# Optimization experiments

Measured on AMD Instinct MI355X. Metric: run time of the kernel, lower is better.

## Reference

```python
import jax, jax.numpy as jnp
import numpy as np

N, M, E, DIM = 100000, 2000, 400000, 128
GIN = 2 * DIM + 3  # gate MLP input width


def _mlp2(x, W1, b1, W2, b2):
    # Linear -> ReLU -> Linear
    return jnp.maximum(x @ W1 + b1, 0.0) @ W2 + b2


def setup_inputs() -> dict:
    key = jax.random.key(0)
    ks = jax.random.split(key, 20)
    s = lambda fan_in: 1.0 / np.sqrt(fan_in)
    inp = {
        "res_feat": jax.random.normal(ks[0], (N, DIM), jnp.float32),
        "meta_feat": jax.random.normal(ks[1], (M, DIM), jnp.float32),
        "sec_ids": jax.random.randint(ks[2], (N,), 0, M),
        "batch_pe_vector": jax.random.normal(ks[3], (N, 3), jnp.float32),
        "batch_meta_2_node_edge": jax.random.randint(ks[4], (2, E), 0, M),
        "batch_meta_2_node_vector": jax.random.normal(ks[5], (E, 3), jnp.float32),
        # gate1 params
        "g1_W1": jax.random.uniform(ks[6], (GIN, DIM), jnp.float32, -s(GIN), s(GIN)),
        "g1_b1": jnp.zeros((DIM,), jnp.float32),
        "g1_W2": jax.random.uniform(ks[7], (DIM, DIM), jnp.float32, -s(DIM), s(DIM)),
        "g1_b2": jnp.zeros((DIM,), jnp.float32),
        # gate2 params
        "g2_W1": jax.random.uniform(ks[8], (GIN, DIM), jnp.float32, -s(GIN), s(GIN)),
        "g2_b1": jnp.zeros((DIM,), jnp.float32),
        "g2_W2": jax.random.uniform(ks[9], (DIM, DIM), jnp.float32, -s(DIM), s(DIM)),
        "g2_b2": jnp.zeros((DIM,), jnp.float32),
        # fuse params
        "f_W1": jax.random.uniform(ks[10], (DIM, DIM), jnp.float32, -s(DIM), s(DIM)),
        "f_b1": jnp.zeros((DIM,), jnp.float32),
        "f_W2": jax.random.uniform(ks[11], (DIM, DIM), jnp.float32, -s(DIM), s(DIM)),
        "f_b2": jnp.zeros((DIM,), jnp.float32),
    }
    return inp


def reference(res_feat, meta_feat, sec_ids, batch_pe_vector,
              batch_meta_2_node_edge, batch_meta_2_node_vector,
              g1_W1, g1_b1, g1_W2, g1_b2,
              g2_W1, g2_b1, g2_W2, g2_b2,
              f_W1, f_b1, f_W2, f_b2):
    n = res_feat.shape[0]
    # gate1: per-node gather of meta features
    meta_broadcast = meta_feat[sec_ids]                       # [N, dim]
    gate1_in = jnp.concatenate([res_feat, meta_broadcast, -batch_pe_vector], axis=-1)
    gate1_w = _mlp2(gate1_in, g1_W1, g1_b1, g1_W2, g1_b2)     # [N, dim]
    # gate2: per-edge gathers
    src, dst = batch_meta_2_node_edge[0], batch_meta_2_node_edge[1]
    meta_add = meta_feat[src]                                 # [E, dim]
    res_b = res_feat[dst]                                     # [E, dim]
    gate2_in = jnp.concatenate([res_b, meta_add, batch_meta_2_node_vector], axis=-1)
    gate2_w = _mlp2(gate2_in, g2_W1, g2_b1, g2_W2, g2_b2)     # [E, dim]
    # scatter_mean over destination nodes
    vals = gate2_w * meta_add
    sums = jax.ops.segment_sum(vals, dst, num_segments=n)
    cnts = jax.ops.segment_sum(jnp.ones((vals.shape[0],), vals.dtype), dst, num_segments=n)
    meta_add_fea = sums / jnp.maximum(cnts, 1.0)[:, None]
    fused = res_feat + gate1_w * meta_broadcast + meta_add_fea
    return _mlp2(fused, f_W1, f_b1, f_W2, f_b2)
```

## Files before the change

kernel.cpp:

```cpp
#include <hip/hip_runtime.h>


typedef short bf16x8 __attribute__((ext_vector_type(8)));
typedef float f32x4  __attribute__((ext_vector_type(4)));

#define XS_PAD 136
#define S_SPLIT 4

__device__ __forceinline__ unsigned short f2bf(float f){
  union { float f; unsigned u; } v; v.f = f;
  return (unsigned short)((v.u + 0x7FFFu + ((v.u >> 16) & 1u)) >> 16);
}
__device__ __forceinline__ unsigned pack2(float a, float b){
  return (unsigned)f2bf(a) | ((unsigned)f2bf(b) << 16);
}
__device__ __forceinline__ float bf2f(unsigned short u){
  union { unsigned u; float f; } v; v.u = ((unsigned)u) << 16; return v.f;
}

__device__ __forceinline__ void mfma_layer(const unsigned short* Xs,
                                           const bf16x8 (&B)[2][4],
                                           int lane, f32x4 (&acc)[4][2]) {
  const int lcol = lane & 15, quad = lane >> 4;
  #pragma unroll
  for (int rg = 0; rg < 4; ++rg) {
    bf16x8 A[4];
    const unsigned short* ab = Xs + (rg*16 + lcol)*XS_PAD + quad*8;
    #pragma unroll
    for (int kk = 0; kk < 4; ++kk) A[kk] = *(const bf16x8*)(ab + kk*32);
    #pragma unroll
    for (int ctl = 0; ctl < 2; ++ctl)
      #pragma unroll
      for (int kk = 0; kk < 4; ++kk)
        acc[rg][ctl] = __builtin_amdgcn_mfma_f32_16x16x32_bf16(
            A[kk], B[ctl][kk], acc[rg][ctl], 0, 0, 0);
  }
}

__device__ __forceinline__ void load_bfrags(const unsigned short* __restrict__ Wt,
                                            int wave, int lane, bf16x8 (&B)[2][4]) {
  const int lcol = lane & 15, quad = lane >> 4;
  #pragma unroll
  for (int ctl = 0; ctl < 2; ++ctl) {
    int col = (wave*2 + ctl)*16 + lcol;
    #pragma unroll
    for (int kk = 0; kk < 4; ++kk)
      B[ctl][kk] = *(const bf16x8*)(Wt + (size_t)col*128 + kk*32 + quad*8);
  }
}

__device__ __forceinline__ void zero_acc(f32x4 (&acc)[4][2]) {
  #pragma unroll
  for (int rg = 0; rg < 4; ++rg)
    #pragma unroll
    for (int ctl = 0; ctl < 2; ++ctl) {
      acc[rg][ctl][0]=0.f; acc[rg][ctl][1]=0.f;
      acc[rg][ctl][2]=0.f; acc[rg][ctl][3]=0.f;
    }
}

struct WPtrs { const float* s[8]; };
__global__ __launch_bounds__(256) void transpose_w8(WPtrs p,
                                                    unsigned short* __restrict__ dstbase) {
  int slab = blockIdx.x >> 4, blk = blockIdx.x & 15;
  const float* W = p.s[slab];
  unsigned short* Wt = dstbase + (size_t)slab*16384;
  int c  = blk*8 + (threadIdx.x >> 5);
  int k0 = (threadIdx.x & 31) * 4;
  unsigned short o[4];
  #pragma unroll
  for (int j = 0; j < 4; ++j) o[j] = f2bf(W[(size_t)(k0 + j)*128 + c]);
  *(uint2*)(Wt + (size_t)c*128 + k0) =
      make_uint2((unsigned)o[0] | ((unsigned)o[1] << 16),
                 (unsigned)o[2] | ((unsigned)o[3] << 16));
}

__global__ __launch_bounds__(256) void prep_mfma(const float* __restrict__ res,
                                                 const float* __restrict__ meta,
                                                 const unsigned short* __restrict__ WAt,
                                                 const unsigned short* __restrict__ WBt,
                                                 float* __restrict__ A2,
                                                 float* __restrict__ M2, int mrows) {
  __shared__ __align__(16) unsigned short Xs[64*XS_PAD];
  const int t = threadIdx.x, lane = t & 63, wave = t >> 6;
  const int quad = lane >> 4, lcol = lane & 15;
  const int tile0 = blockIdx.x * 64;
  const float* X = blockIdx.y ? meta : res;
  const unsigned short* Wt = blockIdx.y ? WBt : WAt;
  float* Y = blockIdx.y ? M2 : A2;
  bf16x8 B[2][4];
  load_bfrags(Wt, wave, lane, B);
  #pragma unroll
  for (int i = 0; i < 8; ++i) {
    int f = t + i*256, row = f >> 5, c4 = f & 31;
    int gr = tile0 + row;
    float4 v = make_float4(0.f,0.f,0.f,0.f);
    if (gr < mrows) v = *(const float4*)(X + (size_t)gr*128 + c4*4);
    *(uint2*)(Xs + row*XS_PAD + c4*4) = make_uint2(pack2(v.x,v.y), pack2(v.z,v.w));
  }
  __syncthreads();
  f32x4 acc[4][2]; zero_acc(acc);
  mfma_layer(Xs, B, lane, acc);
  #pragma unroll
  for (int rg = 0; rg < 4; ++rg)
    #pragma unroll
    for (int ctl = 0; ctl < 2; ++ctl) {
      int col = (wave*2 + ctl)*16 + lcol;
      #pragma unroll
      for (int reg = 0; reg < 4; ++reg) {
        int gr = tile0 + rg*16 + quad*4 + reg;
        if (gr < mrows) Y[(size_t)gr*128 + col] = acc[rg][ctl][reg];
      }
    }
}

__global__ void hist_kernel(const int* __restrict__ dst, int* __restrict__ counts, int E){
  int e = blockIdx.x*256 + threadIdx.x;
  if (e < E) atomicAdd(&counts[dst[e]], 1);
}
__global__ void scan1(const int* __restrict__ counts, int* __restrict__ exoff,
                      int* __restrict__ blocksum, int N){
  __shared__ int s[256];
  int t = threadIdx.x, gid = blockIdx.x*256 + t;
  int v = (gid < N) ? counts[gid] : 0;
  s[t] = v; __syncthreads();
  for (int off = 1; off < 256; off <<= 1){
    int x = (t >= off) ? s[t-off] : 0; __syncthreads();
    s[t] += x; __syncthreads();
  }
  if (gid < N) exoff[gid] = s[t] - v;
  if (t == 255) blocksum[blockIdx.x] = s[255];
}
__global__ void scan2(int* __restrict__ blocksum, int nb){
  __shared__ int s[512];
  int t = threadIdx.x;
  int v = (t < nb) ? blocksum[t] : 0;
  s[t] = v; __syncthreads();
  for (int off = 1; off < 512; off <<= 1){
    int x = (t >= off) ? s[t-off] : 0; __syncthreads();
    s[t] += x; __syncthreads();
  }
  if (t < nb) blocksum[t] = s[t] - v;
}
__global__ void scan3(int* __restrict__ exoff, const int* __restrict__ blockbase,
                      int* __restrict__ cursor, int N){
  int gid = blockIdx.x*256 + threadIdx.x;
  if (gid < N){ int v = exoff[gid] + blockbase[gid >> 8]; exoff[gid] = v; cursor[gid] = v; }
}
__global__ void fill_kernel(const int* __restrict__ dst, int* __restrict__ cursor,
                            int* __restrict__ edge_ids, int E){
  int e = blockIdx.x*256 + threadIdx.x;
  if (e < E){ int p = atomicAdd(&cursor[dst[e]], 1); edge_ids[p] = e; }
}

__global__ __launch_bounds__(256) void edge_mfma(
    const float* __restrict__ A2, const float* __restrict__ M2,
    const float* __restrict__ meta, const float* __restrict__ evec,
    const int* __restrict__ src, const int* __restrict__ edge_ids,
    const int* __restrict__ row_start, const int* __restrict__ counts,
    const float* __restrict__ b1, const float* __restrict__ g2W1full,
    const unsigned short* __restrict__ W2t, const float* __restrict__ b2,
    float* __restrict__ SUM) {
  const int n = blockIdx.x / S_SPLIT, k = blockIdx.x % S_SPLIT;
  const int count = counts[n];
  const int per = (count + S_SPLIT - 1) / S_SPLIT;
  const int lo = k * per;
  int hi = lo + per; if (hi > count) hi = count;
  const int cnt = hi - lo;
  if (cnt <= 0) return;
  const int rs = row_start[n] + lo;

  __shared__ __align__(16) unsigned short Xh[64*XS_PAD];
  __shared__ int srcl[64];
  __shared__ float evl[64*3];
  const int t = threadIdx.x, lane = t & 63, wave = t >> 6;
  const int quad = lane >> 4, lcol = lane & 15;
  const int c0 = (t & 31) * 4, rbase = t >> 5;

  bf16x8 BW2[2][4];
  load_bfrags(W2t, wave, lane, BW2);
  float4 a2v = *(const float4*)(A2 + (size_t)n*128 + c0);
  float4 b1v = *(const float4*)(b1 + c0);
  float4 base = make_float4(a2v.x+b1v.x, a2v.y+b1v.y, a2v.z+b1v.z, a2v.w+b1v.w);
  float4 w0 = *(const float4*)(g2W1full + 256*128 + c0);
  float4 w1 = *(const float4*)(g2W1full + 257*128 + c0);
  float4 w2 = *(const float4*)(g2W1full + 258*128 + c0);
  const int colA = wave*32 + lcol, colB = colA + 16;
  const float b2A = b2[colA], b2B = b2[colB];
  float psA = 0.f, psB = 0.f;

  for (int t0 = 0; t0 < cnt; t0 += 64) {
    __syncthreads();
    if (t < 64) {
      int idx = t0 + t;
      int s = 0; float e0=0.f,e1=0.f,e2=0.f;
      if (idx < cnt) {
        int e = edge_ids[rs + idx];
        s = src[e];
        e0 = evec[(size_t)e*3]; e1 = evec[(size_t)e*3+1]; e2 = evec[(size_t)e*3+2];
      }
      srcl[t] = s; evl[t*3] = e0; evl[t*3+1] = e1; evl[t*3+2] = e2;
    }
    __syncthreads();
    #pragma unroll
    for (int i = 0; i < 8; ++i) {
      int row = rbase + 8*i;
      float4 h = make_float4(0.f,0.f,0.f,0.f);
      if (t0 + row < cnt) {
        int s = srcl[row];
        float4 m = *(const float4*)(M2 + (size_t)s*128 + c0);
        float e0 = evl[row*3], e1 = evl[row*3+1], e2 = evl[row*3+2];
        h.x = fmaxf(base.x + m.x + e0*w0.x + e1*w1.x + e2*w2.x, 0.f);
        h.y = fmaxf(base.y + m.y + e0*w0.y + e1*w1.y + e2*w2.y, 0.f);
        h.z = fmaxf(base.z + m.z + e0*w0.z + e1*w1.z + e2*w2.z, 0.f);
        h.w = fmaxf(base.w + m.w + e0*w0.w + e1*w1.w + e2*w2.w, 0.f);
      }
      *(uint2*)(Xh + row*XS_PAD + c0) = make_uint2(pack2(h.x,h.y), pack2(h.z,h.w));
    }
    __syncthreads();
    f32x4 acc[4][2]; zero_acc(acc);
    mfma_layer(Xh, BW2, lane, acc);
    #pragma unroll
    for (int rg = 0; rg < 4; ++rg)
      #pragma unroll
      for (int reg = 0; reg < 4; ++reg) {
        int rl = rg*16 + quad*4 + reg;
        if (t0 + rl < cnt) {
          int s = srcl[rl];
          psA += (acc[rg][0][reg] + b2A) * meta[(size_t)s*128 + colA];
          psB += (acc[rg][1][reg] + b2B) * meta[(size_t)s*128 + colB];
        }
      }
  }
  psA += __shfl_xor(psA, 16, 64); psA += __shfl_xor(psA, 32, 64);
  psB += __shfl_xor(psB, 16, 64); psB += __shfl_xor(psB, 32, 64);
  if (quad == 0) {
    atomicAdd(&SUM[(size_t)n*128 + colA], psA);
    atomicAdd(&SUM[(size_t)n*128 + colB], psB);
  }
}

__global__ __launch_bounds__(256) void fused_node(
    const float* __restrict__ res, const float* __restrict__ meta,
    const int* __restrict__ sec_ids, const float* __restrict__ pe,
    const float* __restrict__ g1W1full,
    const unsigned short* __restrict__ g1At, const unsigned short* __restrict__ g1Bt,
    const unsigned short* __restrict__ g1W2t, const float* __restrict__ g1b1,
    const float* __restrict__ g1b2,
    const unsigned short* __restrict__ fW1t, const float* __restrict__ fb1v,
    const unsigned short* __restrict__ fW2t, const float* __restrict__ fb2v,
    const float* __restrict__ SUM, const int* __restrict__ counts, int msize,
    float* __restrict__ out, int rows) {
  __shared__ __align__(16) unsigned short Xa[64*XS_PAD];
  __shared__ __align__(16) unsigned short Xm[64*XS_PAD];
  __shared__ int   sids[64];
  __shared__ float pel[64*3];
  __shared__ float inv[64];
  const int t = threadIdx.x, lane = t & 63, wave = t >> 6;
  const int quad = lane >> 4, lcol = lane & 15;
  const int tile0 = blockIdx.x * 64;
  const int c0 = (t & 31) * 4, rbase = t >> 5;

  if (t < 64) {
    int gr = tile0 + t;
    sids[t] = (gr < rows) ? sec_ids[gr] : 0;
    float p0=0.f,p1=0.f,p2=0.f;
    if (gr < rows){ p0=pe[(size_t)gr*3]; p1=pe[(size_t)gr*3+1]; p2=pe[(size_t)gr*3+2]; }
    pel[t*3]=p0; pel[t*3+1]=p1; pel[t*3+2]=p2;
    int c = (gr < rows && gr < msize) ? counts[gr] : 0;
    inv[t] = (c > 0) ? 1.f/(float)c : 0.f;
  }
  const int colA = wave*32 + lcol, colB = colA + 16;
  const float b1A = g1b1[colA],  b1B = g1b1[colB];
  const float b2A = g1b2[colA],  b2B = g1b2[colB];
  const float fb1A = fb1v[colA], fb1B = fb1v[colB];
  const float fb2A = fb2v[colA], fb2B = fb2v[colB];
  const float wA0 = g1W1full[256*128+colA], wA1 = g1W1full[257*128+colA],
              wA2 = g1W1full[258*128+colA];
  const float wB0 = g1W1full[256*128+colB], wB1 = g1W1full[257*128+colB],
              wB2 = g1W1full[258*128+colB];
  bf16x8 BA[2][4], BB[2][4];
  load_bfrags(g1At, wave, lane, BA);
  load_bfrags(g1Bt, wave, lane, BB);
  __syncthreads();

  #pragma unroll
  for (int i = 0; i < 8; ++i) {
    int row = rbase + 8*i;
    int gr = tile0 + row;
    float4 rv = make_float4(0.f,0.f,0.f,0.f);
    float4 mv = make_float4(0.f,0.f,0.f,0.f);
    if (gr < rows) {
      rv = *(const float4*)(res  + (size_t)gr*128 + c0);
      mv = *(const float4*)(meta + (size_t)sids[row]*128 + c0);
    }
    *(uint2*)(Xa + row*XS_PAD + c0) = make_uint2(pack2(rv.x,rv.y), pack2(rv.z,rv.w));
    *(uint2*)(Xm + row*XS_PAD + c0) = make_uint2(pack2(mv.x,mv.y), pack2(mv.z,mv.w));
  }
  __syncthreads();

  f32x4 acc[4][2]; zero_acc(acc);
  mfma_layer(Xa, BA, lane, acc);
  mfma_layer(Xm, BB, lane, acc);
  __syncthreads();
  #pragma unroll
  for (int rg = 0; rg < 4; ++rg)
    #pragma unroll
    for (int reg = 0; reg < 4; ++reg) {
      int row = rg*16 + quad*4 + reg;
      float p0 = pel[row*3], p1 = pel[row*3+1], p2 = pel[row*3+2];
      float vA = acc[rg][0][reg] + b1A - p0*wA0 - p1*wA1 - p2*wA2;
      float vB = acc[rg][1][reg] + b1B - p0*wB0 - p1*wB1 - p2*wB2;
      Xa[row*XS_PAD + colA] = f2bf(fmaxf(vA, 0.f));
      Xa[row*XS_PAD + colB] = f2bf(fmaxf(vB, 0.f));
    }
  __syncthreads();
  bf16x8 B2g[2][4]; load_bfrags(g1W2t, wave, lane, B2g);
  zero_acc(acc);
  mfma_layer(Xa, B2g, lane, acc);
  __syncthreads();
  #pragma unroll
  for (int rg = 0; rg < 4; ++rg)
    #pragma unroll
    for (int reg = 0; reg < 4; ++reg) {
      int row = rg*16 + quad*4 + reg;
      Xa[row*XS_PAD + colA] = f2bf(acc[rg][0][reg] + b2A);
      Xa[row*XS_PAD + colB] = f2bf(acc[rg][1][reg] + b2B);
    }
  __syncthreads();
  #pragma unroll
  for (int i = 0; i < 8; ++i) {
    int row = rbase + 8*i;
    int gr = tile0 + row;
    if (gr < rows) {
      float4 rv = *(const float4*)(res + (size_t)gr*128 + c0);
      uint2 gu = *(const uint2*)(Xa + row*XS_PAD + c0);
      uint2 mu = *(const uint2*)(Xm + row*XS_PAD + c0);
      float g0 = bf2f((unsigned short)(gu.x & 0xFFFF)), g1 = bf2f((unsigned short)(gu.x >> 16));
      float g2 = bf2f((unsigned short)(gu.y & 0xFFFF)), g3 = bf2f((unsigned short)(gu.y >> 16));
      float m0 = bf2f((unsigned short)(mu.x & 0xFFFF)), m1 = bf2f((unsigned short)(mu.x >> 16));
      float m2 = bf2f((unsigned short)(mu.y & 0xFFFF)), m3 = bf2f((unsigned short)(mu.y >> 16));
      float iv = inv[row];
      float s0=0.f,s1=0.f,s2=0.f,s3=0.f;
      if (iv > 0.f) {
        float4 s = *(const float4*)(SUM + (size_t)gr*128 + c0);
        s0 = s.x*iv; s1 = s.y*iv; s2 = s.z*iv; s3 = s.w*iv;
      }
      float f0 = rv.x + g0*m0 + s0, f1 = rv.y + g1*m1 + s1;
      float f2v = rv.z + g2*m2 + s2, f3 = rv.w + g3*m3 + s3;
      *(uint2*)(Xm + row*XS_PAD + c0) = make_uint2(pack2(f0,f1), pack2(f2v,f3));
    }
  }
  __syncthreads();
  bf16x8 BF1[2][4]; load_bfrags(fW1t, wave, lane, BF1);
  zero_acc(acc);
  mfma_layer(Xm, BF1, lane, acc);
  #pragma unroll
  for (int rg = 0; rg < 4; ++rg)
    #pragma unroll
    for (int reg = 0; reg < 4; ++reg) {
      int row = rg*16 + quad*4 + reg;
      Xa[row*XS_PAD + colA] = f2bf(fmaxf(acc[rg][0][reg] + fb1A, 0.f));
      Xa[row*XS_PAD + colB] = f2bf(fmaxf(acc[rg][1][reg] + fb1B, 0.f));
    }
  __syncthreads();
  bf16x8 BF2[2][4]; load_bfrags(fW2t, wave, lane, BF2);
  zero_acc(acc);
  mfma_layer(Xa, BF2, lane, acc);
  #pragma unroll
  for (int rg = 0; rg < 4; ++rg)
    #pragma unroll
    for (int reg = 0; reg < 4; ++reg) {
      int gr = tile0 + rg*16 + quad*4 + reg;
      if (gr < rows) {
        out[(size_t)gr*128 + colA] = acc[rg][0][reg] + fb2A;
        out[(size_t)gr*128 + colB] = acc[rg][1][reg] + fb2B;
      }
    }
}

extern "C" void kernel_launch(void* const* d_in, const int* in_sizes, int n_in,
                              void* d_out, int out_size, void* d_ws, size_t ws_size,
                              hipStream_t stream) {
  const float* res     = (const float*)d_in[0];
  const float* meta    = (const float*)d_in[1];
  const int*   sec_ids = (const int*)  d_in[2];
  const float* pe      = (const float*)d_in[3];
  const int*   edge    = (const int*)  d_in[4];
  const float* evec    = (const float*)d_in[5];
  const float* g1W1 = (const float*)d_in[6];
  const float* g1b1 = (const float*)d_in[7];
  const float* g1W2 = (const float*)d_in[8];
  const float* g1b2 = (const float*)d_in[9];
  const float* g2W1 = (const float*)d_in[10];
  const float* g2b1 = (const float*)d_in[11];
  const float* g2W2 = (const float*)d_in[12];
  const float* g2b2 = (const float*)d_in[13];
  const float* fW1  = (const float*)d_in[14];
  const float* fb1  = (const float*)d_in[15];
  const float* fW2  = (const float*)d_in[16];
  const float* fb2  = (const float*)d_in[17];

  const int N = in_sizes[0] / 128;
  const int M = in_sizes[1] / 128;
  const int E = in_sizes[4] / 2;
  const int* src = edge;
  const int* dst = edge + E;

  float* ws = (float*)d_ws;
  float* A2   = ws;
  float* M2   = A2 + (size_t)M*128;
  float* SUMb = M2 + (size_t)M*128;
  int* counts     = (int*)(SUMb + (size_t)M*128);
  int* row_startp = counts + M;
  int* cursor     = row_startp + M;
  int* blocksum   = cursor + M;
  int* edge_ids   = blocksum + 512;
  uintptr_t wp = (uintptr_t)(edge_ids + E);
  wp = (wp + 15) & ~(uintptr_t)15;
  unsigned short* Wt = (unsigned short*)wp;
  unsigned short* W_g1A  = Wt + 0*16384;
  unsigned short* W_g1B  = Wt + 1*16384;
  unsigned short* W_g1W2 = Wt + 2*16384;
  unsigned short* W_g2A  = Wt + 3*16384;
  unsigned short* W_g2B  = Wt + 4*16384;
  unsigned short* W_g2W2 = Wt + 5*16384;
  unsigned short* W_fW1  = Wt + 6*16384;
  unsigned short* W_fW2  = Wt + 7*16384;
  float* out = (float*)d_out;

  hipMemsetAsync(counts, 0, (size_t)M*sizeof(int), stream);
  hipMemsetAsync(SUMb, 0, (size_t)M*128*sizeof(float), stream);

  WPtrs p;
  p.s[0] = g1W1;            p.s[1] = g1W1 + 128*128;  p.s[2] = g1W2;
  p.s[3] = g2W1;            p.s[4] = g2W1 + 128*128;  p.s[5] = g2W2;
  p.s[6] = fW1;             p.s[7] = fW2;
  transpose_w8<<<128, 256, 0, stream>>>(p, Wt);

  const int nbMt = (M + 63) / 64;
  const int nbN  = (N + 63) / 64;
  const int nbE  = (E + 255) / 256;
  const int nbS  = (M + 255) / 256;

  prep_mfma<<<dim3(nbMt, 2), 256, 0, stream>>>(res, meta, W_g2A, W_g2B, A2, M2, M);

  hist_kernel<<<nbE, 256, 0, stream>>>(dst, counts, E);
  scan1<<<nbS, 256, 0, stream>>>(counts, row_startp, blocksum, M);
  scan2<<<1, 512, 0, stream>>>(blocksum, nbS);
  scan3<<<nbS, 256, 0, stream>>>(row_startp, blocksum, cursor, M);
  fill_kernel<<<nbE, 256, 0, stream>>>(dst, cursor, edge_ids, E);

  edge_mfma<<<M*S_SPLIT, 256, 0, stream>>>(A2, M2, meta, evec, src, edge_ids,
                                           row_startp, counts, g2b1, g2W1,
                                           W_g2W2, g2b2, SUMb);

  fused_node<<<nbN, 256, 0, stream>>>(res, meta, sec_ids, pe, g1W1,
                                      W_g1A, W_g1B, W_g1W2, g1b1, g1b2,
                                      W_fW1, fb1, W_fW2, fb2,
                                      SUMb, counts, M, out, N);
}
```

Measured before the change: 396.3 us.

## Merge launches, pack edge data in CSR fill, and shrink fused_node LDS

The memsets are folded into the weight-transpose kernel, the prep GEMM and histogram run in one launch, and the three-kernel scan becomes a single-block scan, which cuts launch count. The fill kernel now writes src index and edge vector as a packed float4 in CSR order, so edge_mfma drops the edge_ids indirection and prefetches the next tile's edge data. fused_node uses one LDS tile instead of two and loads weight fragments as needed, aiming for lower LDS and register use and higher occupancy. The cost is that the epilogue rereads meta, res and SUM from global memory with scattered scalar loads.

```diff
diff --git a/kernel.cpp b/kernel.cpp
--- a/kernel.cpp
+++ b/kernel.cpp
@@ -13,9 +13,6 @@
 }
 __device__ __forceinline__ unsigned pack2(float a, float b){
   return (unsigned)f2bf(a) | ((unsigned)f2bf(b) << 16);
-}
-__device__ __forceinline__ float bf2f(unsigned short u){
-  union { unsigned u; float f; } v; v.u = ((unsigned)u) << 16; return v.f;
 }
 
 __device__ __forceinline__ void mfma_layer(const unsigned short* Xs,
@@ -61,7 +58,9 @@
 
 struct WPtrs { const float* s[8]; };
 __global__ __launch_bounds__(256) void transpose_w8(WPtrs p,
-                                                    unsigned short* __restrict__ dstbase) {
+                                                    unsigned short* __restrict__ dstbase,
+                                                    float* __restrict__ SUM,
+                                                    int* __restrict__ counts, int M) {
   int slab = blockIdx.x >> 4, blk = blockIdx.x & 15;
   const float* W = p.s[slab];
   unsigned short* Wt = dstbase + (size_t)slab*16384;
@@ -73,21 +72,34 @@
   *(uint2*)(Wt + (size_t)c*128 + k0) =
       make_uint2((unsigned)o[0] | ((unsigned)o[1] << 16),
                  (unsigned)o[2] | ((unsigned)o[3] << 16));
-}
-
-__global__ __launch_bounds__(256) void prep_mfma(const float* __restrict__ res,
-                                                 const float* __restrict__ meta,
-                                                 const unsigned short* __restrict__ WAt,
-                                                 const unsigned short* __restrict__ WBt,
-                                                 float* __restrict__ A2,
-                                                 float* __restrict__ M2, int mrows) {
+  int tid = blockIdx.x*256 + threadIdx.x;
+  int tot = gridDim.x*256;
+  float4 z = make_float4(0.f,0.f,0.f,0.f);
+  for (int i = tid; i < M*32; i += tot) ((float4*)SUM)[i] = z;
+  for (int i = tid; i < M; i += tot) counts[i] = 0;
+}
+
+__global__ __launch_bounds__(256) void prep_and_hist(
+    const float* __restrict__ res, const float* __restrict__ meta,
+    const unsigned short* __restrict__ WAt, const unsigned short* __restrict__ WBt,
+    const float* __restrict__ b1,
+    float* __restrict__ A2, float* __restrict__ M2, int mrows, int nbPrep,
+    const int* __restrict__ dst, int* __restrict__ counts, int E) {
+  if ((int)blockIdx.x >= nbPrep) {
+    int e = ((int)blockIdx.x - nbPrep)*256 + threadIdx.x;
+    if (e < E) atomicAdd(&counts[dst[e]], 1);
+    return;
+  }
   __shared__ __align__(16) unsigned short Xs[64*XS_PAD];
   const int t = threadIdx.x, lane = t & 63, wave = t >> 6;
   const int quad = lane >> 4, lcol = lane & 15;
-  const int tile0 = blockIdx.x * 64;
-  const float* X = blockIdx.y ? meta : res;
-  const unsigned short* Wt = blockIdx.y ? WBt : WAt;
-  float* Y = blockIdx.y ? M2 : A2;
+  const int half = nbPrep >> 1;
+  const int yy = ((int)blockIdx.x >= half) ? 1 : 0;
+  const int bx = (int)blockIdx.x - yy*half;
+  const int tile0 = bx * 64;
+  const float* X = yy ? meta : res;
+  const unsigned short* Wt = yy ? WBt : WAt;
+  float* Y = yy ? M2 : A2;
   bf16x8 B[2][4];
   load_bfrags(Wt, wave, lane, B);
   #pragma unroll
@@ -106,59 +118,60 @@
     #pragma unroll
     for (int ctl = 0; ctl < 2; ++ctl) {
       int col = (wave*2 + ctl)*16 + lcol;
+      float badd = 0.f;
+      if (!yy) badd = b1[col];
       #pragma unroll
       for (int reg = 0; reg < 4; ++reg) {
         int gr = tile0 + rg*16 + quad*4 + reg;
-        if (gr < mrows) Y[(size_t)gr*128 + col] = acc[rg][ctl][reg];
+        if (gr < mrows) Y[(size_t)gr*128 + col] = acc[rg][ctl][reg] + badd;
       }
     }
 }
 
-__global__ void hist_kernel(const int* __restrict__ dst, int* __restrict__ counts, int E){
+__global__ __launch_bounds__(1024) void scan_all(const int* __restrict__ counts,
+                                                 int* __restrict__ row_start,
+                                                 int* __restrict__ cursor, int M) {
+  __shared__ int s[1024];
+  __shared__ int carry_s;
+  const int t = threadIdx.x;
+  if (t == 0) carry_s = 0;
+  __syncthreads();
+  for (int base = 0; base < M; base += 2048) {
+    int i0 = base + 2*t, i1 = i0 + 1;
+    int c0 = (i0 < M) ? counts[i0] : 0;
+    int c1 = (i1 < M) ? counts[i1] : 0;
+    int pair = c0 + c1;
+    s[t] = pair; __syncthreads();
+    for (int off = 1; off < 1024; off <<= 1) {
+      int x = (t >= off) ? s[t-off] : 0; __syncthreads();
+      s[t] += x; __syncthreads();
+    }
+    int carry = carry_s;
+    int excl = carry + s[t] - pair;
+    if (i0 < M) { row_start[i0] = excl;       cursor[i0] = excl; }
+    if (i1 < M) { row_start[i1] = excl + c0;  cursor[i1] = excl + c0; }
+    __syncthreads();
+    if (t == 1023) carry_s = carry + s[1023];
+    __syncthreads();
+  }
+}
+
+__global__ void fill_kernel(const int* __restrict__ dst, const int* __restrict__ src,
+                            const float* __restrict__ evec, int* __restrict__ cursor,
+                            float4* __restrict__ edata, int E) {
   int e = blockIdx.x*256 + threadIdx.x;
-  if (e < E) atomicAdd(&counts[dst[e]], 1);
-}
-__global__ void scan1(const int* __restrict__ counts, int* __restrict__ exoff,
-                      int* __restrict__ blocksum, int N){
-  __shared__ int s[256];
-  int t = threadIdx.x, gid = blockIdx.x*256 + t;
-  int v = (gid < N) ? counts[gid] : 0;
-  s[t] = v; __syncthreads();
-  for (int off = 1; off < 256; off <<= 1){
-    int x = (t >= off) ? s[t-off] : 0; __syncthreads();
-    s[t] += x; __syncthreads();
-  }
-  if (gid < N) exoff[gid] = s[t] - v;
-  if (t == 255) blocksum[blockIdx.x] = s[255];
-}
-__global__ void scan2(int* __restrict__ blocksum, int nb){
-  __shared__ int s[512];
-  int t = threadIdx.x;
-  int v = (t < nb) ? blocksum[t] : 0;
-  s[t] = v; __syncthreads();
-  for (int off = 1; off < 512; off <<= 1){
-    int x = (t >= off) ? s[t-off] : 0; __syncthreads();
-    s[t] += x; __syncthreads();
-  }
-  if (t < nb) blocksum[t] = s[t] - v;
-}
-__global__ void scan3(int* __restrict__ exoff, const int* __restrict__ blockbase,
-                      int* __restrict__ cursor, int N){
-  int gid = blockIdx.x*256 + threadIdx.x;
-  if (gid < N){ int v = exoff[gid] + blockbase[gid >> 8]; exoff[gid] = v; cursor[gid] = v; }
-}
-__global__ void fill_kernel(const int* __restrict__ dst, int* __restrict__ cursor,
-                            int* __restrict__ edge_ids, int E){
-  int e = blockIdx.x*256 + threadIdx.x;
-  if (e < E){ int p = atomicAdd(&cursor[dst[e]], 1); edge_ids[p] = e; }
+  if (e < E) {
+    int p = atomicAdd(&cursor[dst[e]], 1);
+    edata[p] = make_float4(__int_as_float(src[e]),
+                           evec[(size_t)e*3], evec[(size_t)e*3+1], evec[(size_t)e*3+2]);
+  }
 }
 
 __global__ __launch_bounds__(256) void edge_mfma(
     const float* __restrict__ A2, const float* __restrict__ M2,
-    const float* __restrict__ meta, const float* __restrict__ evec,
-    const int* __restrict__ src, const int* __restrict__ edge_ids,
+    const float* __restrict__ meta, const float4* __restrict__ edata,
     const int* __restrict__ row_start, const int* __restrict__ counts,
-    const float* __restrict__ b1, const float* __restrict__ g2W1full,
+    const float* __restrict__ g2W1full,
     const unsigned short* __restrict__ W2t, const float* __restrict__ b2,
     float* __restrict__ SUM) {
   const int n = blockIdx.x / S_SPLIT, k = blockIdx.x % S_SPLIT;
@@ -172,16 +185,17 @@
 
   __shared__ __align__(16) unsigned short Xh[64*XS_PAD];
   __shared__ int srcl[64];
-  __shared__ float evl[64*3];
+  __shared__ float evl[192];
   const int t = threadIdx.x, lane = t & 63, wave = t >> 6;
   const int quad = lane >> 4, lcol = lane & 15;
   const int c0 = (t & 31) * 4, rbase = t >> 5;
 
+  float4 ed = make_float4(0.f,0.f,0.f,0.f);
+  if (t < 64 && t < cnt) ed = edata[rs + t];
+
   bf16x8 BW2[2][4];
   load_bfrags(W2t, wave, lane, BW2);
-  float4 a2v = *(const float4*)(A2 + (size_t)n*128 + c0);
-  float4 b1v = *(const float4*)(b1 + c0);
-  float4 base = make_float4(a2v.x+b1v.x, a2v.y+b1v.y, a2v.z+b1v.z, a2v.w+b1v.w);
+  float4 base = *(const float4*)(A2 + (size_t)n*128 + c0);
   float4 w0 = *(const float4*)(g2W1full + 256*128 + c0);
   float4 w1 = *(const float4*)(g2W1full + 257*128 + c0);
   float4 w2 = *(const float4*)(g2W1full + 258*128 + c0);
@@ -190,16 +204,13 @@
   float psA = 0.f, psB = 0.f;
 
   for (int t0 = 0; t0 < cnt; t0 += 64) {
-    __syncthreads();
+    if (t0) __syncthreads();
     if (t < 64) {
-      int idx = t0 + t;
-      int s = 0; float e0=0.f,e1=0.f,e2=0.f;
-      if (idx < cnt) {
-        int e = edge_ids[rs + idx];
-        s = src[e];
-        e0 = evec[(size_t)e*3]; e1 = evec[(size_t)e*3+1]; e2 = evec[(size_t)e*3+2];
-      }
-      srcl[t] = s; evl[t*3] = e0; evl[t*3+1] = e1; evl[t*3+2] = e2;
+      srcl[t] = __float_as_int(ed.x);
+      evl[3*t] = ed.y; evl[3*t+1] = ed.z; evl[3*t+2] = ed.w;
+      int idx = t0 + 64 + t;
+      ed = make_float4(0.f,0.f,0.f,0.f);
+      if (idx < cnt) ed = edata[rs + idx];
     }
     __syncthreads();
     #pragma unroll
@@ -209,7 +220,7 @@
       if (t0 + row < cnt) {
         int s = srcl[row];
         float4 m = *(const float4*)(M2 + (size_t)s*128 + c0);
-        float e0 = evl[row*3], e1 = evl[row*3+1], e2 = evl[row*3+2];
+        float e0 = evl[3*row], e1 = evl[3*row+1], e2 = evl[3*row+2];
         h.x = fmaxf(base.x + m.x + e0*w0.x + e1*w1.x + e2*w2.x, 0.f);
         h.y = fmaxf(base.y + m.y + e0*w0.y + e1*w1.y + e2*w2.y, 0.f);
         h.z = fmaxf(base.z + m.z + e0*w0.z + e1*w1.z + e2*w2.z, 0.f);
@@ -251,132 +262,131 @@
     const unsigned short* __restrict__ fW2t, const float* __restrict__ fb2v,
     const float* __restrict__ SUM, const int* __restrict__ counts, int msize,
     float* __restrict__ out, int rows) {
-  __shared__ __align__(16) unsigned short Xa[64*XS_PAD];
-  __shared__ __align__(16) unsigned short Xm[64*XS_PAD];
+  __shared__ __align__(16) unsigned short Xs[64*XS_PAD];
   __shared__ int   sids[64];
-  __shared__ float pel[64*3];
+  __shared__ float pel[192];
   __shared__ float inv[64];
   const int t = threadIdx.x, lane = t & 63, wave = t >> 6;
   const int quad = lane >> 4, lcol = lane & 15;
   const int tile0 = blockIdx.x * 64;
   const int c0 = (t & 31) * 4, rbase = t >> 5;
+  const int colA = wave*32 + lcol, colB = colA + 16;
 
   if (t < 64) {
     int gr = tile0 + t;
     sids[t] = (gr < rows) ? sec_ids[gr] : 0;
     float p0=0.f,p1=0.f,p2=0.f;
     if (gr < rows){ p0=pe[(size_t)gr*3]; p1=pe[(size_t)gr*3+1]; p2=pe[(size_t)gr*3+2]; }
-    pel[t*3]=p0; pel[t*3+1]=p1; pel[t*3+2]=p2;
+    pel[3*t]=p0; pel[3*t+1]=p1; pel[3*t+2]=p2;
     int c = (gr < rows && gr < msize) ? counts[gr] : 0;
     inv[t] = (c > 0) ? 1.f/(float)c : 0.f;
   }
-  const int colA = wave*32 + lcol, colB = colA + 16;
-  const float b1A = g1b1[colA],  b1B = g1b1[colB];
-  const float b2A = g1b2[colA],  b2B = g1b2[colB];
-  const float fb1A = fb1v[colA], fb1B = fb1v[colB];
-  const float fb2A = fb2v[colA], fb2B = fb2v[colB];
-  const float wA0 = g1W1full[256*128+colA], wA1 = g1W1full[257*128+colA],
-              wA2 = g1W1full[258*128+colA];
-  const float wB0 = g1W1full[256*128+colB], wB1 = g1W1full[257*128+colB],
-              wB2 = g1W1full[258*128+colB];
-  bf16x8 BA[2][4], BB[2][4];
-  load_bfrags(g1At, wave, lane, BA);
-  load_bfrags(g1Bt, wave, lane, BB);
-  __syncthreads();
-
+  bf16x8 BF[2][4];
+  load_bfrags(g1At, wave, lane, BF);
   #pragma unroll
   for (int i = 0; i < 8; ++i) {
-    int row = rbase + 8*i;
-    int gr = tile0 + row;
-    float4 rv = make_float4(0.f,0.f,0.f,0.f);
-    float4 mv = make_float4(0.f,0.f,0.f,0.f);
-    if (gr < rows) {
-      rv = *(const float4*)(res  + (size_t)gr*128 + c0);
-      mv = *(const float4*)(meta + (size_t)sids[row]*128 + c0);
-    }
-    *(uint2*)(Xa + row*XS_PAD + c0) = make_uint2(pack2(rv.x,rv.y), pack2(rv.z,rv.w));
-    *(uint2*)(Xm + row*XS_PAD + c0) = make_uint2(pack2(mv.x,mv.y), pack2(mv.z,mv.w));
-  }
-  __syncthreads();
-
+    int row = rbase + 8*i, gr = tile0 + row;
+    float4 v = make_float4(0.f,0.f,0.f,0.f);
+    if (gr < rows) v = *(const float4*)(res + (size_t)gr*128 + c0);
+    *(uint2*)(Xs + row*XS_PAD + c0) = make_uint2(pack2(v.x,v.y), pack2(v.z,v.w));
+  }
+  __syncthreads();
   f32x4 acc[4][2]; zero_acc(acc);
-  mfma_layer(Xa, BA, lane, acc);
-  mfma_layer(Xm, BB, lane, acc);
-  __syncthreads();
-  #pragma unroll
-  for (int rg = 0; rg < 4; ++rg)
-    #pragma unroll
-    for (int reg = 0; reg < 4; ++reg) {
-      int row = rg*16 + quad*4 + reg;
-      float p0 = pel[row*3], p1 = pel[row*3+1], p2 = pel[row*3+2];
-      float vA = acc[rg][0][reg] + b1A - p0*wA0 - p1*wA1 - p2*wA2;
-      float vB = acc[rg][1][reg] + b1B - p0*wB0 - p1*wB1 - p2*wB2;
-      Xa[row*XS_PAD + colA] = f2bf(fmaxf(vA, 0.f));
-      Xa[row*XS_PAD + colB] = f2bf(fmaxf(vB, 0.f));
-    }
-  __syncthreads();
-  bf16x8 B2g[2][4]; load_bfrags(g1W2t, wave, lane, B2g);
+  mfma_layer(Xs, BF, lane, acc);
+  load_bfrags(g1Bt, wave, lane, BF);
+  __syncthreads();
+  #pragma unroll
+  for (int i = 0; i < 8; ++i) {
+    int row = rbase + 8*i, gr = tile0 + row;
+    float4 v = make_float4(0.f,0.f,0.f,0.f);
+    if (gr < rows) v = *(const float4*)(meta + (size_t)sids[row]*128 + c0);
+    *(uint2*)(Xs + row*XS_PAD + c0) = make_uint2(pack2(v.x,v.y), pack2(v.z,v.w));
+  }
+  __syncthreads();
+  mfma_layer(Xs, BF, lane, acc);
+  load_bfrags(g1W2t, wave, lane, BF);
+  __syncthreads();
+  {
+    const float b1A = g1b1[colA], b1B = g1b1[colB];
+    const float wA0 = g1W1full[256*128+colA], wA1 = g1W1full[257*128+colA],
+                wA2 = g1W1full[258*128+colA];
+    const float wB0 = g1W1full[256*128+colB], wB1 = g1W1full[257*128+colB],
+                wB2 = g1W1full[258*128+colB];
+    #pragma unroll
+    for (int rg = 0; rg < 4; ++rg)
+      #pragma unroll
+      for (int reg = 0; reg < 4; ++reg) {
+        int row = rg*16 + quad*4 + reg;
+        float p0 = pel[3*row], p1 = pel[3*row+1], p2 = pel[3*row+2];
+        float vA = acc[rg][0][reg] + b1A - p0*wA0 - p1*wA1 - p2*wA2;
+        float vB = acc[rg][1][reg] + b1B - p0*wB0 - p1*wB1 - p2*wB2;
+        Xs[row*XS_PAD + colA] = f2bf(fmaxf(vA, 0.f));
+        Xs[row*XS_PAD + colB] = f2bf(fmaxf(vB, 0.f));
+      }
+  }
+  __syncthreads();
   zero_acc(acc);
-  mfma_layer(Xa, B2g, lane, acc);
-  __syncthreads();
-  #pragma unroll
-  for (int rg = 0; rg < 4; ++rg)
-    #pragma unroll
-    for (int reg = 0; reg < 4; ++reg) {
-      int row = rg*16 + quad*4 + reg;
-      Xa[row*XS_PAD + colA] = f2bf(acc[rg][0][reg] + b2A);
-      Xa[row*XS_PAD + colB] = f2bf(acc[rg][1][reg] + b2B);
-    }
-  __syncthreads();
-  #pragma unroll
-  for (int i = 0; i < 8; ++i) {
-    int row = rbase + 8*i;
-    int gr = tile0 + row;
-    if (gr < rows) {
-      float4 rv = *(const float4*)(res + (size_t)gr*128 + c0);
-      uint2 gu = *(const uint2*)(Xa + row*XS_PAD + c0);
-      uint2 mu = *(const uint2*)(Xm + row*XS_PAD + c0);
-      float g0 = bf2f((unsigned short)(gu.x & 0xFFFF)), g1 = bf2f((unsigned short)(gu.x >> 16));
-      float g2 = bf2f((unsigned short)(gu.y & 0xFFFF)), g3 = bf2f((unsigned short)(gu.y >> 16));
-      float m0 = bf2f((unsigned short)(mu.x & 0xFFFF)), m1 = bf2f((unsigned short)(mu.x >> 16));
-      float m2 = bf2f((unsigned short)(mu.y & 0xFFFF)), m3 = bf2f((unsigned short)(mu.y >> 16));
-      float iv = inv[row];
-      float s0=0.f,s1=0.f,s2=0.f,s3=0.f;
-      if (iv > 0.f) {
-        float4 s = *(const float4*)(SUM + (size_t)gr*128 + c0);
-        s0 = s.x*iv; s1 = s.y*iv; s2 = s.z*iv; s3 = s.w*iv;
-      }
-      float f0 = rv.x + g0*m0 + s0, f1 = rv.y + g1*m1 + s1;
-      float f2v = rv.z + g2*m2 + s2, f3 = rv.w + g3*m3 + s3;
-      *(uint2*)(Xm + row*XS_PAD + c0) = make_uint2(pack2(f0,f1), pack2(f2v,f3));
-    }
-  }
-  __syncthreads();
-  bf16x8 BF1[2][4]; load_bfrags(fW1t, wave, lane, BF1);
+  mfma_layer(Xs, BF, lane, acc);
+  load_bfrags(fW1t, wave, lane, BF);
+  __syncthreads();
+  {
+    const float b2A = g1b2[colA], b2B = g1b2[colB];
+    #pragma unroll
+    for (int rg = 0; rg < 4; ++rg)
+      #pragma unroll
+      for (int reg = 0; reg < 4; ++reg) {
+        int row = rg*16 + quad*4 + reg, gr = tile0 + row;
+        unsigned short oA = 0, oB = 0;
+        if (gr < rows) {
+          int sid = sids[row];
+          float gA = acc[rg][0][reg] + b2A, gB = acc[rg][1][reg] + b2B;
+          float mA = meta[(size_t)sid*128 + colA], mB = meta[(size_t)sid*128 + colB];
+          float rA = res[(size_t)gr*128 + colA],  rB = res[(size_t)gr*128 + colB];
+          float iv = inv[row];
+          float sA = 0.f, sB = 0.f;
+          if (iv > 0.f) {
+            sA = SUM[(size_t)gr*128 + colA] * iv;
+            sB = SUM[(size_t)gr*128 + colB] * iv;
+          }
+          oA = f2bf(rA + gA*mA + sA);
+          oB = f2bf(rB + gB*mB + sB);
+        }
+        Xs[row*XS_PAD + colA] = oA;
+        Xs[row*XS_PAD + colB] = oB;
+      }
+  }
+  __syncthreads();
   zero_acc(acc);
-  mfma_layer(Xm, BF1, lane, acc);
-  #pragma unroll
-  for (int rg = 0; rg < 4; ++rg)
-    #pragma unroll
-    for (int reg = 0; reg < 4; ++reg) {
-      int row = rg*16 + quad*4 + reg;
-      Xa[row*XS_PAD + colA] = f2bf(fmaxf(acc[rg][0][reg] + fb1A, 0.f));
-      Xa[row*XS_PAD + colB] = f2bf(fmaxf(acc[rg][1][reg] + fb1B, 0.f));
-    }
-  __syncthreads();
-  bf16x8 BF2[2][4]; load_bfrags(fW2t, wave, lane, BF2);
+  mfma_layer(Xs, BF, lane, acc);
+  load_bfrags(fW2t, wave, lane, BF);
+  __syncthreads();
+  {
+    const float fb1A = fb1v[colA], fb1B = fb1v[colB];
+    #pragma unroll
+    for (int rg = 0; rg < 4; ++rg)
+      #pragma unroll
+      for (int reg = 0; reg < 4; ++reg) {
+        int row = rg*16 + quad*4 + reg;
+        Xs[row*XS_PAD + colA] = f2bf(fmaxf(acc[rg][0][reg] + fb1A, 0.f));
+        Xs[row*XS_PAD + colB] = f2bf(fmaxf(acc[rg][1][reg] + fb1B, 0.f));
+      }
+  }
+  __syncthreads();
   zero_acc(acc);
-  mfma_layer(Xa, BF2, lane, acc);
-  #pragma unroll
-  for (int rg = 0; rg < 4; ++rg)
-    #pragma unroll
-    for (int reg = 0; reg < 4; ++reg) {
-      int gr = tile0 + rg*16 + quad*4 + reg;
-      if (gr < rows) {
-        out[(size_t)gr*128 + colA] = acc[rg][0][reg] + fb2A;
-        out[(size_t)gr*128 + colB] = acc[rg][1][reg] + fb2B;
-      }
-    }
+  mfma_layer(Xs, BF, lane, acc);
+  {
+    const float fb2A = fb2v[colA], fb2B = fb2v[colB];
+    #pragma unroll
+    for (int rg = 0; rg < 4; ++rg)
+      #pragma unroll
+      for (int reg = 0; reg < 4; ++reg) {
+        int gr = tile0 + rg*16 + quad*4 + reg;
+        if (gr < rows) {
+          out[(size_t)gr*128 + colA] = acc[rg][0][reg] + fb2A;
+          out[(size_t)gr*128 + colB] = acc[rg][1][reg] + fb2B;
+        }
+      }
+  }
 }
 
 extern "C" void kernel_launch(void* const* d_in, const int* in_sizes, int n_in,
@@ -414,9 +424,10 @@
   int* counts     = (int*)(SUMb + (size_t)M*128);
   int* row_startp = counts + M;
   int* cursor     = row_startp + M;
-  int* blocksum   = cursor + M;
-  int* edge_ids   = blocksum + 512;
-  uintptr_t wp = (uintptr_t)(edge_ids + E);
+  uintptr_t ap = (uintptr_t)(cursor + M);
+  ap = (ap + 15) & ~(uintptr_t)15;
+  float4* edata = (float4*)ap;
+  uintptr_t wp = (uintptr_t)(edata + E);
   wp = (wp + 15) & ~(uintptr_t)15;
   unsigned short* Wt = (unsigned short*)wp;
   unsigned short* W_g1A  = Wt + 0*16384;
@@ -429,32 +440,23 @@
   unsigned short* W_fW2  = Wt + 7*16384;
   float* out = (float*)d_out;
 
-  hipMemsetAsync(counts, 0, (size_t)M*sizeof(int), stream);
-  hipMemsetAsync(SUMb, 0, (size_t)M*128*sizeof(float), stream);
-
   WPtrs p;
   p.s[0] = g1W1;            p.s[1] = g1W1 + 128*128;  p.s[2] = g1W2;
   p.s[3] = g2W1;            p.s[4] = g2W1 + 128*128;  p.s[5] = g2W2;
   p.s[6] = fW1;             p.s[7] = fW2;
-  transpose_w8<<<128, 256, 0, stream>>>(p, Wt);
 
   const int nbMt = (M + 63) / 64;
   const int nbN  = (N + 63) / 64;
   const int nbE  = (E + 255) / 256;
-  const int nbS  = (M + 255) / 256;
-
-  prep_mfma<<<dim3(nbMt, 2), 256, 0, stream>>>(res, meta, W_g2A, W_g2B, A2, M2, M);
-
-  hist_kernel<<<nbE, 256, 0, stream>>>(dst, counts, E);
-  scan1<<<nbS, 256, 0, stream>>>(counts, row_startp, blocksum, M);
-  scan2<<<1, 512, 0, stream>>>(blocksum, nbS);
-  scan3<<<nbS, 256, 0, stream>>>(row_startp, blocksum, cursor, M);
-  fill_kernel<<<nbE, 256, 0, stream>>>(dst, cursor, edge_ids, E);
-
-  edge_mfma<<<M*S_SPLIT, 256, 0, stream>>>(A2, M2, meta, evec, src, edge_ids,
-                                           row_startp, counts, g2b1, g2W1,
-                                           W_g2W2, g2b2, SUMb);
-
+  const int nbPrep = 2*nbMt;
+
+  transpose_w8<<<128, 256, 0, stream>>>(p, Wt, SUMb, counts, M);
+  prep_and_hist<<<nbPrep + nbE, 256, 0, stream>>>(res, meta, W_g2A, W_g2B, g2b1,
+                                                  A2, M2, M, nbPrep, dst, counts, E);
+  scan_all<<<1, 1024, 0, stream>>>(counts, row_startp, cursor, M);
+  fill_kernel<<<nbE, 256, 0, stream>>>(dst, src, evec, cursor, edata, E);
+  edge_mfma<<<M*S_SPLIT, 256, 0, stream>>>(A2, M2, meta, edata, row_startp, counts,
+                                           g2W1, W_g2W2, g2b2, SUMb);
   fused_node<<<nbN, 256, 0, stream>>>(res, meta, sec_ids, pe, g1W1,
                                       W_g1A, W_g1B, W_g1W2, g1b1, g1b2,
                                       W_fW1, fb1, W_fW2, fb2,
```

After: 406.0 us. +2.4%, slower.
